# Optimization experiments

Measured on AMD Instinct MI355X. Metric: run time of the kernel, lower is better.

Reference implementation:

```python
import jax, jax.numpy as jnp
import numpy as np

B, L, D = 1, 4096, 1024
N_AR, N_DIFF, D_HEAD = 8, 8, 64
H = N_AR + N_DIFF
ROPE_BASE = 10000.0


def rotate_half(x):
    x1, x2 = jnp.split(x, 2, axis=-1)
    return jnp.concatenate([-x2, x1], axis=-1)


def rope_cos_sin(seq_len, d_head):
    inv_freq = 1.0 / (ROPE_BASE ** (jnp.arange(0, d_head, 2, dtype=jnp.float32) / d_head))
    t = jnp.arange(seq_len, dtype=jnp.float32)
    freqs = t[:, None] * inv_freq[None, :]          # [L, d_head//2]
    emb = jnp.concatenate([freqs, freqs], axis=-1)  # [L, d_head]
    return jnp.cos(emb), jnp.sin(emb)


def setup_inputs() -> dict:
    key = jax.random.key(0)
    ks = jax.random.split(key, 5)
    return {
        "hidden_states": jax.random.normal(ks[0], (B, L, D), dtype=jnp.float32),
        "Wq": jax.random.normal(ks[1], (D, H * D_HEAD), dtype=jnp.float32) * 0.02,
        "Wk": jax.random.normal(ks[2], (D, H * D_HEAD), dtype=jnp.float32) * 0.02,
        "Wv": jax.random.normal(ks[3], (D, H * D_HEAD), dtype=jnp.float32) * 0.02,
        "Wo": jax.random.normal(ks[4], (H * D_HEAD, D), dtype=jnp.float32) * 0.02,
    }


def _attend(q, k, v, mask):
    # q,k,v: [B, h, L, d]; mask: [L, L] additive
    scale = D_HEAD ** -0.5
    scores = jnp.einsum("bhqd,bhkd->bhqk", q, k) * scale + mask
    attn = jax.nn.softmax(scores.astype(jnp.float32), axis=-1).astype(q.dtype)
    return jnp.einsum("bhqk,bhkd->bhqd", attn, v)


def reference(hidden_states, Wq, Wk, Wv, Wo):
    b, l, _ = hidden_states.shape

    def heads(x, W):
        return (x @ W).reshape(b, l, H, D_HEAD).transpose(0, 2, 1, 3)  # [B,H,L,d]

    q = heads(hidden_states, Wq)
    k = heads(hidden_states, Wk)
    v = heads(hidden_states, Wv)

    cos, sin = rope_cos_sin(l, D_HEAD)  # [L, d]
    q = q * cos + rotate_half(q) * sin
    k = k * cos + rotate_half(k) * sin

    neg_inf = jnp.finfo(jnp.float32).min
    causal = jnp.where(jnp.tril(jnp.ones((l, l), dtype=bool)), 0.0, -jnp.inf).astype(jnp.float32)

    out_ar = _attend(q[:, :N_AR], k[:, :N_AR], v[:, :N_AR], causal)
    out_diff = _attend(q[:, N_AR:], k[:, N_AR:], v[:, N_AR:], jnp.zeros((l, l), jnp.float32))

    out = jnp.concatenate([out_ar, out_diff], axis=1)          # [B,H,L,d]
    out = out.transpose(0, 2, 1, 3).reshape(b, l, H * D_HEAD)  # [B,L,H*d]
    return out @ Wo
```

## Files before the change

kernel.cpp:

```cpp
#include <hip/hip_runtime.h>

#define LSEQ 4096
#define DMODEL 1024
#define HTOT 16
#define NAR 8
#define DHEAD 64
#define QKVS 3072

typedef unsigned short u16;
typedef unsigned int u32;
typedef __attribute__((ext_vector_type(8))) short bf16x8;
typedef __attribute__((ext_vector_type(4))) short bf16x4;
typedef __attribute__((ext_vector_type(4))) float f32x4;

typedef __attribute__((address_space(1))) void gvoid;
typedef __attribute__((address_space(3))) void lvoid;

__device__ __forceinline__ void cp16(const void* g, void* l) {
    __builtin_amdgcn_global_load_lds((gvoid*)(void*)g, (lvoid*)l, 16, 0, 0);
}

__device__ __forceinline__ float bfs(u16 v) { return __uint_as_float((u32)v << 16); }
__device__ __forceinline__ u16 f2bf(float f) {
    u32 x = __float_as_uint(f);
    return (u16)((x + 0x7fffu + ((x >> 16) & 1u)) >> 16);
}
__device__ __forceinline__ u32 pack2(float a, float b) {
    return (u32)f2bf(a) | ((u32)f2bf(b) << 16);
}

__global__ __launch_bounds__(256) void transp_cvt3(
    const float* __restrict__ Wq, const float* __restrict__ Wk,
    const float* __restrict__ Wv, u16* __restrict__ D)
{
    __shared__ u16 T[64][72];
    const float* S = (blockIdx.z == 0) ? Wq : ((blockIdx.z == 1) ? Wk : Wv);
    u16* Dz = D + (size_t)blockIdx.z * 1024 * 1024;
    const int tid = threadIdx.x;
    const int bx = blockIdx.x, by = blockIdx.y;
#pragma unroll
    for (int i = 0; i < 4; ++i) {
        int id = tid + i * 256;
        int fr = id >> 4, fc = id & 15;
        float4 v = *(const float4*)(S + (size_t)(by * 64 + fr) * 1024 + bx * 64 + fc * 4);
        T[fc * 4 + 0][fr] = f2bf(v.x);
        T[fc * 4 + 1][fr] = f2bf(v.y);
        T[fc * 4 + 2][fr] = f2bf(v.z);
        T[fc * 4 + 3][fr] = f2bf(v.w);
    }
    __syncthreads();
#pragma unroll
    for (int i = 0; i < 2; ++i) {
        int id = tid + i * 256;
        int c = id >> 3, g = id & 7;
        *(uint4*)(Dz + (size_t)(bx * 64 + c) * 1024 + by * 64 + g * 8) = *(const uint4*)&T[c][g * 8];
    }
}

__global__ __launch_bounds__(256) void transp_cvt(
    const float* __restrict__ S, u16* __restrict__ D)
{
    __shared__ u16 T[64][72];
    const int tid = threadIdx.x;
    const int bx = blockIdx.x, by = blockIdx.y;
#pragma unroll
    for (int i = 0; i < 4; ++i) {
        int id = tid + i * 256;
        int fr = id >> 4, fc = id & 15;
        float4 v = *(const float4*)(S + (size_t)(by * 64 + fr) * 1024 + bx * 64 + fc * 4);
        T[fc * 4 + 0][fr] = f2bf(v.x);
        T[fc * 4 + 1][fr] = f2bf(v.y);
        T[fc * 4 + 2][fr] = f2bf(v.z);
        T[fc * 4 + 3][fr] = f2bf(v.w);
    }
    __syncthreads();
#pragma unroll
    for (int i = 0; i < 2; ++i) {
        int id = tid + i * 256;
        int c = id >> 3, g = id & 7;
        *(uint4*)(D + (size_t)(bx * 64 + c) * 1024 + by * 64 + g * 8) = *(const uint4*)&T[c][g * 8];
    }
}

__global__ __launch_bounds__(256) void gemm_qkv(
    const float* __restrict__ A, const u16* __restrict__ Bt, u16* __restrict__ C)
{
    __shared__ u16 As[2][128][40];
    __shared__ u16 Bs[2][128][32];
    const int tid = threadIdx.x;
    const int lane = tid & 63, w = tid >> 6;
    const int col = lane & 15, quad = lane >> 4;
    const int bm = blockIdx.y << 7, bn = blockIdx.x << 7;
    const int wm = (w & 1) << 6, wn = (w >> 1) << 6;
    const int sr = lane >> 2, sc = (lane & 3) << 3;
    const int ar0 = tid >> 2, ag = (tid & 3) << 3;
    const f32x4 zero = {0.f, 0.f, 0.f, 0.f};
    f32x4 acc[4][4];
#pragma unroll
    for (int i = 0; i < 4; ++i)
#pragma unroll
        for (int j = 0; j < 4; ++j) acc[i][j] = zero;

    {
#pragma unroll
        for (int i = 0; i < 2; ++i)
            cp16(Bt + (size_t)(bn + w * 32 + i * 16 + sr) * 1024 + sc, &Bs[0][w * 32 + i * 16][0]);
        float4 a0[2], a1[2];
#pragma unroll
        for (int it = 0; it < 2; ++it) {
            const float* ap = A + (size_t)(bm + ar0 + it * 64) * 1024 + ag;
            a0[it] = *(const float4*)ap;
            a1[it] = *(const float4*)(ap + 4);
        }
#pragma unroll
        for (int it = 0; it < 2; ++it) {
            uint4 pk;
            pk.x = pack2(a0[it].x, a0[it].y); pk.y = pack2(a0[it].z, a0[it].w);
            pk.z = pack2(a1[it].x, a1[it].y); pk.w = pack2(a1[it].z, a1[it].w);
            *(uint4*)&As[0][ar0 + it * 64][ag] = pk;
        }
    }

    for (int kc = 0; kc < 32; ++kc) {
        const int cur = kc & 1, nxt = cur ^ 1;
        __syncthreads();
        const bool pre = (kc + 1 < 32);
        float4 a0[2], a1[2];
        if (pre) {
            const int k1 = (kc + 1) * 32;
#pragma unroll
            for (int i = 0; i < 2; ++i)
                cp16(Bt + (size_t)(bn + w * 32 + i * 16 + sr) * 1024 + k1 + sc,
                     &Bs[nxt][w * 32 + i * 16][0]);
#pragma unroll
            for (int it = 0; it < 2; ++it) {
                const float* ap = A + (size_t)(bm + ar0 + it * 64) * 1024 + k1 + ag;
                a0[it] = *(const float4*)ap;
                a1[it] = *(const float4*)(ap + 4);
            }
        }
        bf16x8 af[4], bfr[4];
#pragma unroll
        for (int i = 0; i < 4; ++i) af[i] = *(const bf16x8*)&As[cur][wm + i * 16 + col][quad * 8];
#pragma unroll
        for (int j = 0; j < 4; ++j) bfr[j] = *(const bf16x8*)&Bs[cur][wn + j * 16 + col][quad * 8];
#pragma unroll
        for (int i = 0; i < 4; ++i)
#pragma unroll
            for (int j = 0; j < 4; ++j)
                acc[i][j] = __builtin_amdgcn_mfma_f32_16x16x32_bf16(af[i], bfr[j], acc[i][j], 0, 0, 0);
        if (pre) {
#pragma unroll
            for (int it = 0; it < 2; ++it) {
                uint4 pk;
                pk.x = pack2(a0[it].x, a0[it].y); pk.y = pack2(a0[it].z, a0[it].w);
                pk.z = pack2(a1[it].x, a1[it].y); pk.w = pack2(a1[it].z, a1[it].w);
                *(uint4*)&As[nxt][ar0 + it * 64][ag] = pk;
            }
        }
    }
#pragma unroll
    for (int i = 0; i < 4; ++i)
#pragma unroll
        for (int j = 0; j < 4; ++j)
#pragma unroll
            for (int r = 0; r < 4; ++r)
                C[(size_t)(bm + wm + i * 16 + quad * 4 + r) * QKVS + bn + wn + j * 16 + col] =
                    f2bf(acc[i][j][r]);
}

__global__ __launch_bounds__(256) void gemm_out(
    const u16* __restrict__ A, const u16* __restrict__ Bt, float* __restrict__ C)
{
    __shared__ u16 As[2][128][32];
    __shared__ u16 Bs[2][128][32];
    const int tid = threadIdx.x;
    const int lane = tid & 63, w = tid >> 6;
    const int col = lane & 15, quad = lane >> 4;
    const int bm = blockIdx.y << 7, bn = blockIdx.x << 7;
    const int wm = (w & 1) << 6, wn = (w >> 1) << 6;
    const int sr = lane >> 2, sc = (lane & 3) << 3;
    const f32x4 zero = {0.f, 0.f, 0.f, 0.f};
    f32x4 acc[4][4];
#pragma unroll
    for (int i = 0; i < 4; ++i)
#pragma unroll
        for (int j = 0; j < 4; ++j) acc[i][j] = zero;

#pragma unroll
    for (int i = 0; i < 2; ++i) {
        const int r0 = w * 32 + i * 16;
        cp16(A  + (size_t)(bm + r0 + sr) * 1024 + sc, &As[0][r0][0]);
        cp16(Bt + (size_t)(bn + r0 + sr) * 1024 + sc, &Bs[0][r0][0]);
    }

    for (int kc = 0; kc < 32; ++kc) {
        const int cur = kc & 1, nxt = cur ^ 1;
        __syncthreads();
        if (kc + 1 < 32) {
            const int k1 = (kc + 1) * 32;
#pragma unroll
            for (int i = 0; i < 2; ++i) {
                const int r0 = w * 32 + i * 16;
                cp16(A  + (size_t)(bm + r0 + sr) * 1024 + k1 + sc, &As[nxt][r0][0]);
                cp16(Bt + (size_t)(bn + r0 + sr) * 1024 + k1 + sc, &Bs[nxt][r0][0]);
            }
        }
        bf16x8 af[4], bfr[4];
#pragma unroll
        for (int i = 0; i < 4; ++i) af[i] = *(const bf16x8*)&As[cur][wm + i * 16 + col][quad * 8];
#pragma unroll
        for (int j = 0; j < 4; ++j) bfr[j] = *(const bf16x8*)&Bs[cur][wn + j * 16 + col][quad * 8];
#pragma unroll
        for (int i = 0; i < 4; ++i)
#pragma unroll
            for (int j = 0; j < 4; ++j)
                acc[i][j] = __builtin_amdgcn_mfma_f32_16x16x32_bf16(af[i], bfr[j], acc[i][j], 0, 0, 0);
    }
#pragma unroll
    for (int i = 0; i < 4; ++i)
#pragma unroll
        for (int j = 0; j < 4; ++j)
#pragma unroll
            for (int r = 0; r < 4; ++r)
                C[(size_t)(bm + wm + i * 16 + quad * 4 + r) * 1024 + bn + wn + j * 16 + col] =
                    acc[i][j][r];
}

__global__ __launch_bounds__(256) void rope_kernel(u16* __restrict__ QKV)
{
    const int idx = blockIdx.x * 256 + threadIdx.x;
    const int i = idx & 31;
    const int h = (idx >> 5) & 15;
    const int t = idx >> 9;
    const float inv = __expf((float)i * -0.2878231366242557f);
    float s, c;
    __sincosf((float)t * inv, &s, &c);
    const size_t base = (size_t)t * QKVS + h * DHEAD + i;
    const float qs = 0.18033688011112042f;

    float q1 = bfs(QKV[base]), q2 = bfs(QKV[base + 32]);
    QKV[base]      = f2bf((q1 * c - q2 * s) * qs);
    QKV[base + 32] = f2bf((q2 * c + q1 * s) * qs);

    const size_t kb = base + 1024;
    float k1 = bfs(QKV[kb]), k2 = bfs(QKV[kb + 32]);
    QKV[kb]      = f2bf(k1 * c - k2 * s);
    QKV[kb + 32] = f2bf(k2 * c + k1 * s);
}

__global__ __launch_bounds__(256) void attn_mfma(
    const u16* __restrict__ QKV, u16* __restrict__ AO)
{
    __shared__ u16 Ks[2][64][64];
    __shared__ u16 Vt[2][64][72];
    const int bid = blockIdx.x;
    int h, qt;
    if (bid < 512) { h = 8 + (bid & 7); qt = bid >> 3; }
    else {
        int i = bid - 512; h = i & 7; int j = i >> 3;
        qt = (j & 1) ? (63 - (j >> 1)) : (j >> 1);
    }
    const bool causal = (h < NAR);
    const int tid = threadIdx.x;
    const int w = tid >> 6, lane = tid & 63;
    const int col = lane & 15, quad = lane >> 4;
    const int qb = qt * 64;
    const int qrow = qb + w * 16 + col;

    bf16x8 qf[2];
#pragma unroll
    for (int ks = 0; ks < 2; ++ks)
        qf[ks] = *(const bf16x8*)(QKV + (size_t)qrow * QKVS + h * DHEAD + ks * 32 + quad * 8);

    bf16x4 ones;
    ones[0] = (short)0x3F80; ones[1] = (short)0x3F80;
    ones[2] = (short)0x3F80; ones[3] = (short)0x3F80;

    const f32x4 zero = {0.f, 0.f, 0.f, 0.f};
    f32x4 O[5];
#pragma unroll
    for (int nd = 0; nd < 5; ++nd) O[nd] = zero;

    const int nch = causal ? (qt + 1) : (LSEQ / 64);
    const int kv_kp = tid & 31, kv_dg = tid >> 5;
    const int krow = lane >> 3;
    const int kcb = (lane & 7) ^ krow;
    const u16* kbase = QKV + (size_t)krow * QKVS + 1024 + h * DHEAD + kcb * 8;

    {
#pragma unroll
        for (int i = 0; i < 2; ++i)
            cp16(kbase + (size_t)((i * 4 + w) * 8) * QKVS, &Ks[0][(i * 4 + w) * 8][0]);
        const u16* vp = QKV + (size_t)(kv_kp * 2) * QKVS + 2048 + h * DHEAD + kv_dg * 8;
        bf16x8 v0 = *(const bf16x8*)vp;
        bf16x8 v1 = *(const bf16x8*)(vp + QKVS);
#pragma unroll
        for (int j = 0; j < 8; ++j)
            *(u32*)&Vt[0][kv_dg * 8 + j][kv_kp * 2] = (u32)(u16)v0[j] | ((u32)(u16)v1[j] << 16);
    }

    for (int ch = 0; ch < nch; ++ch) {
        const int cur = ch & 1, nxt = cur ^ 1;
        __syncthreads();
        const bool pre = (ch + 1 < nch);
        bf16x8 v0 = {}, v1 = {};
        if (pre) {
            const int c1 = (ch + 1) * 64;
#pragma unroll
            for (int i = 0; i < 2; ++i)
                cp16(kbase + (size_t)(c1 + (i * 4 + w) * 8) * QKVS, &Ks[nxt][(i * 4 + w) * 8][0]);
            const u16* vp = QKV + (size_t)(c1 + kv_kp * 2) * QKVS + 2048 + h * DHEAD + kv_dg * 8;
            v0 = *(const bf16x8*)vp;
            v1 = *(const bf16x8*)(vp + QKVS);
        }

        f32x4 st[4];
#pragma unroll
        for (int jn = 0; jn < 4; ++jn) st[jn] = zero;
#pragma unroll
        for (int jn = 0; jn < 4; ++jn)
#pragma unroll
            for (int ks = 0; ks < 2; ++ks) {
                bf16x8 kf = *(const bf16x8*)&Ks[cur][jn * 16 + col][((ks * 4 + quad) ^ (col & 7)) * 8];
                st[jn] = __builtin_amdgcn_mfma_f32_16x16x32_bf16(kf, qf[ks], st[jn], 0, 0, 0);
            }
        if (causal && ch * 64 + 63 > qb + w * 16) {
#pragma unroll
            for (int jn = 0; jn < 4; ++jn) {
                int kk = ch * 64 + jn * 16 + quad * 4;
#pragma unroll
                for (int r = 0; r < 4; ++r)
                    if (kk + r > qrow) st[jn][r] = -1e30f;
            }
        }
        bf16x4 pf[4];
#pragma unroll
        for (int jn = 0; jn < 4; ++jn) {
            pf[jn][0] = (short)f2bf(__builtin_amdgcn_exp2f(st[jn][0]));
            pf[jn][1] = (short)f2bf(__builtin_amdgcn_exp2f(st[jn][1]));
            pf[jn][2] = (short)f2bf(__builtin_amdgcn_exp2f(st[jn][2]));
            pf[jn][3] = (short)f2bf(__builtin_amdgcn_exp2f(st[jn][3]));
        }
#pragma unroll
        for (int nd = 0; nd < 4; ++nd)
#pragma unroll
            for (int jn = 0; jn < 4; ++jn) {
                bf16x4 vtf = *(const bf16x4*)&Vt[cur][nd * 16 + col][jn * 16 + quad * 4];
                O[nd] = __builtin_amdgcn_mfma_f32_16x16x16bf16_1k(vtf, pf[jn], O[nd], 0, 0, 0);
            }
#pragma unroll
        for (int jn = 0; jn < 4; ++jn)
            O[4] = __builtin_amdgcn_mfma_f32_16x16x16bf16_1k(ones, pf[jn], O[4], 0, 0, 0);

        if (pre) {
#pragma unroll
            for (int j = 0; j < 8; ++j)
                *(u32*)&Vt[nxt][kv_dg * 8 + j][kv_kp * 2] =
                    (u32)(u16)v0[j] | ((u32)(u16)v1[j] << 16);
        }
    }
    const float inv = 1.f / O[4][0];
#pragma unroll
    for (int nd = 0; nd < 4; ++nd) {
        ushort4 ov;
        ov.x = f2bf(O[nd][0] * inv);
        ov.y = f2bf(O[nd][1] * inv);
        ov.z = f2bf(O[nd][2] * inv);
        ov.w = f2bf(O[nd][3] * inv);
        *(ushort4*)(AO + (size_t)qrow * 1024 + h * DHEAD + nd * 16 + quad * 4) = ov;
    }
}

extern "C" void kernel_launch(void* const* d_in, const int* in_sizes, int n_in,
                              void* d_out, int out_size, void* d_ws, size_t ws_size,
                              hipStream_t stream)
{
    const float* X  = (const float*)d_in[0];
    const float* Wq = (const float*)d_in[1];
    const float* Wk = (const float*)d_in[2];
    const float* Wv = (const float*)d_in[3];
    const float* Wo = (const float*)d_in[4];
    float* out = (float*)d_out;

    u16* Wt  = (u16*)d_ws;
    u16* AOb = (u16*)d_ws;
    u16* QKV = (u16*)d_ws + (size_t)4 * 1024 * 1024;
    u16* Wot = QKV;

    transp_cvt3<<<dim3(16, 16, 3), 256, 0, stream>>>(Wq, Wk, Wv, Wt);
    gemm_qkv<<<dim3(24, 32), 256, 0, stream>>>(X, Wt, QKV);
    rope_kernel<<<(LSEQ * HTOT * 32) / 256, 256, 0, stream>>>(QKV);
    attn_mfma<<<1024, 256, 0, stream>>>(QKV, AOb);
    transp_cvt<<<dim3(16, 16), 256, 0, stream>>>(Wo, Wot);
    gemm_out<<<dim3(8, 32), 256, 0, stream>>>(AOb, Wot, out);
}
```

Before: 275.1 us.

## Double attention tile to 128 queries and 128 keys per block

The attention kernel now handles 128 query rows per block, with each wave doing two 16-row sub-tiles, and 128 keys per chunk. Each K/V fragment loaded from LDS is therefore reused across two query sub-tiles, which halves the number of blocks and the K/V global traffic per query. V is transposed with perm byte-shuffles, and probabilities are packed to bf16 by truncation instead of round-to-nearest. In exchange the kernel uses more registers and LDS, has half as many blocks (512 on a large GPU), and the causal blocks become coarser with more imbalance.

```diff
diff --git a/kernel.cpp b/kernel.cpp
--- a/kernel.cpp
+++ b/kernel.cpp
@@ -12,6 +12,7 @@
 typedef __attribute__((ext_vector_type(8))) short bf16x8;
 typedef __attribute__((ext_vector_type(4))) short bf16x4;
 typedef __attribute__((ext_vector_type(4))) float f32x4;
+typedef __attribute__((ext_vector_type(4))) unsigned int u32x4;
 
 typedef __attribute__((address_space(1))) void gvoid;
 typedef __attribute__((address_space(3))) void lvoid;
@@ -27,6 +28,9 @@
 }
 __device__ __forceinline__ u32 pack2(float a, float b) {
     return (u32)f2bf(a) | ((u32)f2bf(b) << 16);
+}
+__device__ __forceinline__ u32 packtr(float lo, float hi) {
+    return __builtin_amdgcn_perm(__float_as_uint(hi), __float_as_uint(lo), 0x07060302u);
 }
 
 __global__ __launch_bounds__(256) void transp_cvt3(
@@ -252,123 +256,156 @@
 __global__ __launch_bounds__(256) void attn_mfma(
     const u16* __restrict__ QKV, u16* __restrict__ AO)
 {
-    __shared__ u16 Ks[2][64][64];
-    __shared__ u16 Vt[2][64][72];
+    __shared__ u16 Ks[2][128][64];
+    __shared__ u16 Vt[2][64][136];
     const int bid = blockIdx.x;
     int h, qt;
-    if (bid < 512) { h = 8 + (bid & 7); qt = bid >> 3; }
-    else {
-        int i = bid - 512; h = i & 7; int j = i >> 3;
-        qt = (j & 1) ? (63 - (j >> 1)) : (j >> 1);
-    }
+    if (bid < 256) { h = 8 + (bid & 7); qt = bid >> 3; }
+    else { int i = bid - 256; h = i & 7; qt = 31 - (i >> 3); }
     const bool causal = (h < NAR);
     const int tid = threadIdx.x;
     const int w = tid >> 6, lane = tid & 63;
     const int col = lane & 15, quad = lane >> 4;
-    const int qb = qt * 64;
-    const int qrow = qb + w * 16 + col;
-
-    bf16x8 qf[2];
-#pragma unroll
-    for (int ks = 0; ks < 2; ++ks)
-        qf[ks] = *(const bf16x8*)(QKV + (size_t)qrow * QKVS + h * DHEAD + ks * 32 + quad * 8);
+    const int qb = qt * 128;
+    const int qr0 = qb + w * 32 + col;
+    const int qr1 = qr0 + 16;
+
+    bf16x8 qf[2][2];
+#pragma unroll
+    for (int s = 0; s < 2; ++s)
+#pragma unroll
+        for (int ks = 0; ks < 2; ++ks)
+            qf[s][ks] = *(const bf16x8*)(QKV + (size_t)(qr0 + s * 16) * QKVS +
+                                         h * DHEAD + ks * 32 + quad * 8);
 
     bf16x4 ones;
     ones[0] = (short)0x3F80; ones[1] = (short)0x3F80;
     ones[2] = (short)0x3F80; ones[3] = (short)0x3F80;
 
     const f32x4 zero = {0.f, 0.f, 0.f, 0.f};
-    f32x4 O[5];
-#pragma unroll
-    for (int nd = 0; nd < 5; ++nd) O[nd] = zero;
-
-    const int nch = causal ? (qt + 1) : (LSEQ / 64);
-    const int kv_kp = tid & 31, kv_dg = tid >> 5;
+    f32x4 O[2][5];
+#pragma unroll
+    for (int s = 0; s < 2; ++s)
+#pragma unroll
+        for (int nd = 0; nd < 5; ++nd) O[s][nd] = zero;
+
+    const int nch = causal ? (qt + 1) : (LSEQ / 128);
     const int krow = lane >> 3;
     const int kcb = (lane & 7) ^ krow;
     const u16* kbase = QKV + (size_t)krow * QKVS + 1024 + h * DHEAD + kcb * 8;
+    const u16* vbase = QKV + (size_t)(lane * 2) * QKVS + 2048 + h * DHEAD + w * 16;
 
     {
 #pragma unroll
-        for (int i = 0; i < 2; ++i)
+        for (int i = 0; i < 4; ++i)
             cp16(kbase + (size_t)((i * 4 + w) * 8) * QKVS, &Ks[0][(i * 4 + w) * 8][0]);
-        const u16* vp = QKV + (size_t)(kv_kp * 2) * QKVS + 2048 + h * DHEAD + kv_dg * 8;
-        bf16x8 v0 = *(const bf16x8*)vp;
-        bf16x8 v1 = *(const bf16x8*)(vp + QKVS);
-#pragma unroll
-        for (int j = 0; j < 8; ++j)
-            *(u32*)&Vt[0][kv_dg * 8 + j][kv_kp * 2] = (u32)(u16)v0[j] | ((u32)(u16)v1[j] << 16);
+        u32x4 A0 = *(u32x4*)(vbase);
+        u32x4 A1 = *(u32x4*)(vbase + 8);
+        u32x4 B0 = *(u32x4*)(vbase + QKVS);
+        u32x4 B1 = *(u32x4*)(vbase + QKVS + 8);
+#pragma unroll
+        for (int j = 0; j < 4; ++j) {
+            *(u32*)&Vt[0][w * 16 + 2 * j][lane * 2]     = __builtin_amdgcn_perm(B0[j], A0[j], 0x05040100u);
+            *(u32*)&Vt[0][w * 16 + 2 * j + 1][lane * 2] = __builtin_amdgcn_perm(B0[j], A0[j], 0x07060302u);
+            *(u32*)&Vt[0][w * 16 + 8 + 2 * j][lane * 2]     = __builtin_amdgcn_perm(B1[j], A1[j], 0x05040100u);
+            *(u32*)&Vt[0][w * 16 + 8 + 2 * j + 1][lane * 2] = __builtin_amdgcn_perm(B1[j], A1[j], 0x07060302u);
+        }
     }
 
     for (int ch = 0; ch < nch; ++ch) {
         const int cur = ch & 1, nxt = cur ^ 1;
         __syncthreads();
         const bool pre = (ch + 1 < nch);
-        bf16x8 v0 = {}, v1 = {};
+        u32x4 A0 = {}, A1 = {}, B0 = {}, B1 = {};
         if (pre) {
-            const int c1 = (ch + 1) * 64;
-#pragma unroll
-            for (int i = 0; i < 2; ++i)
-                cp16(kbase + (size_t)(c1 + (i * 4 + w) * 8) * QKVS, &Ks[nxt][(i * 4 + w) * 8][0]);
-            const u16* vp = QKV + (size_t)(c1 + kv_kp * 2) * QKVS + 2048 + h * DHEAD + kv_dg * 8;
-            v0 = *(const bf16x8*)vp;
-            v1 = *(const bf16x8*)(vp + QKVS);
-        }
-
-        f32x4 st[4];
-#pragma unroll
-        for (int jn = 0; jn < 4; ++jn) st[jn] = zero;
-#pragma unroll
-        for (int jn = 0; jn < 4; ++jn)
-#pragma unroll
-            for (int ks = 0; ks < 2; ++ks) {
-                bf16x8 kf = *(const bf16x8*)&Ks[cur][jn * 16 + col][((ks * 4 + quad) ^ (col & 7)) * 8];
-                st[jn] = __builtin_amdgcn_mfma_f32_16x16x32_bf16(kf, qf[ks], st[jn], 0, 0, 0);
-            }
-        if (causal && ch * 64 + 63 > qb + w * 16) {
-#pragma unroll
-            for (int jn = 0; jn < 4; ++jn) {
-                int kk = ch * 64 + jn * 16 + quad * 4;
-#pragma unroll
-                for (int r = 0; r < 4; ++r)
-                    if (kk + r > qrow) st[jn][r] = -1e30f;
-            }
-        }
-        bf16x4 pf[4];
-#pragma unroll
-        for (int jn = 0; jn < 4; ++jn) {
-            pf[jn][0] = (short)f2bf(__builtin_amdgcn_exp2f(st[jn][0]));
-            pf[jn][1] = (short)f2bf(__builtin_amdgcn_exp2f(st[jn][1]));
-            pf[jn][2] = (short)f2bf(__builtin_amdgcn_exp2f(st[jn][2]));
-            pf[jn][3] = (short)f2bf(__builtin_amdgcn_exp2f(st[jn][3]));
-        }
-#pragma unroll
-        for (int nd = 0; nd < 4; ++nd)
-#pragma unroll
-            for (int jn = 0; jn < 4; ++jn) {
-                bf16x4 vtf = *(const bf16x4*)&Vt[cur][nd * 16 + col][jn * 16 + quad * 4];
-                O[nd] = __builtin_amdgcn_mfma_f32_16x16x16bf16_1k(vtf, pf[jn], O[nd], 0, 0, 0);
-            }
-#pragma unroll
-        for (int jn = 0; jn < 4; ++jn)
-            O[4] = __builtin_amdgcn_mfma_f32_16x16x16bf16_1k(ones, pf[jn], O[4], 0, 0, 0);
+            const size_t c1 = (size_t)(ch + 1) * 128;
+#pragma unroll
+            for (int i = 0; i < 4; ++i)
+                cp16(kbase + (c1 + (i * 4 + w) * 8) * QKVS, &Ks[nxt][(i * 4 + w) * 8][0]);
+            const u16* vp = vbase + c1 * QKVS;
+            A0 = *(u32x4*)(vp);
+            A1 = *(u32x4*)(vp + 8);
+            B0 = *(u32x4*)(vp + QKVS);
+            B1 = *(u32x4*)(vp + QKVS + 8);
+        }
+
+#pragma unroll
+        for (int hf = 0; hf < 2; ++hf) {
+            f32x4 st[2][4];
+#pragma unroll
+            for (int s = 0; s < 2; ++s)
+#pragma unroll
+                for (int jj = 0; jj < 4; ++jj) st[s][jj] = zero;
+#pragma unroll
+            for (int jj = 0; jj < 4; ++jj)
+#pragma unroll
+                for (int ks = 0; ks < 2; ++ks) {
+                    bf16x8 kf = *(const bf16x8*)&Ks[cur][(hf * 4 + jj) * 16 + col]
+                                                    [((ks * 4 + quad) ^ (col & 7)) * 8];
+                    st[0][jj] = __builtin_amdgcn_mfma_f32_16x16x32_bf16(kf, qf[0][ks], st[0][jj], 0, 0, 0);
+                    st[1][jj] = __builtin_amdgcn_mfma_f32_16x16x32_bf16(kf, qf[1][ks], st[1][jj], 0, 0, 0);
+                }
+            if (causal && ch == qt) {
+#pragma unroll
+                for (int jj = 0; jj < 4; ++jj) {
+                    const int kk = ch * 128 + (hf * 4 + jj) * 16 + quad * 4;
+#pragma unroll
+                    for (int r = 0; r < 4; ++r) {
+                        if (kk + r > qr0) st[0][jj][r] = -1e30f;
+                        if (kk + r > qr1) st[1][jj][r] = -1e30f;
+                    }
+                }
+            }
+            bf16x4 pf[2][4];
+#pragma unroll
+            for (int s = 0; s < 2; ++s)
+#pragma unroll
+                for (int jj = 0; jj < 4; ++jj) {
+                    u32 lo = packtr(__builtin_amdgcn_exp2f(st[s][jj][0]),
+                                    __builtin_amdgcn_exp2f(st[s][jj][1]));
+                    u32 hi = packtr(__builtin_amdgcn_exp2f(st[s][jj][2]),
+                                    __builtin_amdgcn_exp2f(st[s][jj][3]));
+                    u32* p = (u32*)&pf[s][jj];
+                    p[0] = lo; p[1] = hi;
+                }
+#pragma unroll
+            for (int nd = 0; nd < 4; ++nd)
+#pragma unroll
+                for (int jj = 0; jj < 4; ++jj) {
+                    bf16x4 vtf = *(const bf16x4*)&Vt[cur][nd * 16 + col][(hf * 4 + jj) * 16 + quad * 4];
+                    O[0][nd] = __builtin_amdgcn_mfma_f32_16x16x16bf16_1k(vtf, pf[0][jj], O[0][nd], 0, 0, 0);
+                    O[1][nd] = __builtin_amdgcn_mfma_f32_16x16x16bf16_1k(vtf, pf[1][jj], O[1][nd], 0, 0, 0);
+                }
+#pragma unroll
+            for (int jj = 0; jj < 4; ++jj) {
+                O[0][4] = __builtin_amdgcn_mfma_f32_16x16x16bf16_1k(ones, pf[0][jj], O[0][4], 0, 0, 0);
+                O[1][4] = __builtin_amdgcn_mfma_f32_16x16x16bf16_1k(ones, pf[1][jj], O[1][4], 0, 0, 0);
+            }
+        }
 
         if (pre) {
 #pragma unroll
-            for (int j = 0; j < 8; ++j)
-                *(u32*)&Vt[nxt][kv_dg * 8 + j][kv_kp * 2] =
-                    (u32)(u16)v0[j] | ((u32)(u16)v1[j] << 16);
-        }
-    }
-    const float inv = 1.f / O[4][0];
-#pragma unroll
-    for (int nd = 0; nd < 4; ++nd) {
-        ushort4 ov;
-        ov.x = f2bf(O[nd][0] * inv);
-        ov.y = f2bf(O[nd][1] * inv);
-        ov.z = f2bf(O[nd][2] * inv);
-        ov.w = f2bf(O[nd][3] * inv);
-        *(ushort4*)(AO + (size_t)qrow * 1024 + h * DHEAD + nd * 16 + quad * 4) = ov;
+            for (int j = 0; j < 4; ++j) {
+                *(u32*)&Vt[nxt][w * 16 + 2 * j][lane * 2]     = __builtin_amdgcn_perm(B0[j], A0[j], 0x05040100u);
+                *(u32*)&Vt[nxt][w * 16 + 2 * j + 1][lane * 2] = __builtin_amdgcn_perm(B0[j], A0[j], 0x07060302u);
+                *(u32*)&Vt[nxt][w * 16 + 8 + 2 * j][lane * 2]     = __builtin_amdgcn_perm(B1[j], A1[j], 0x05040100u);
+                *(u32*)&Vt[nxt][w * 16 + 8 + 2 * j + 1][lane * 2] = __builtin_amdgcn_perm(B1[j], A1[j], 0x07060302u);
+            }
+        }
+    }
+#pragma unroll
+    for (int s = 0; s < 2; ++s) {
+        const float inv = 1.f / O[s][4][0];
+        const int qrow = qr0 + s * 16;
+#pragma unroll
+        for (int nd = 0; nd < 4; ++nd) {
+            ushort4 ov;
+            ov.x = f2bf(O[s][nd][0] * inv);
+            ov.y = f2bf(O[s][nd][1] * inv);
+            ov.z = f2bf(O[s][nd][2] * inv);
+            ov.w = f2bf(O[s][nd][3] * inv);
+            *(ushort4*)(AO + (size_t)qrow * 1024 + h * DHEAD + nd * 16 + quad * 4) = ov;
+        }
     }
 }
 
@@ -391,7 +428,7 @@
     transp_cvt3<<<dim3(16, 16, 3), 256, 0, stream>>>(Wq, Wk, Wv, Wt);
     gemm_qkv<<<dim3(24, 32), 256, 0, stream>>>(X, Wt, QKV);
     rope_kernel<<<(LSEQ * HTOT * 32) / 256, 256, 0, stream>>>(QKV);
-    attn_mfma<<<1024, 256, 0, stream>>>(QKV, AOb);
+    attn_mfma<<<512, 256, 0, stream>>>(QKV, AOb);
     transp_cvt<<<dim3(16, 16), 256, 0, stream>>>(Wo, Wot);
     gemm_out<<<dim3(8, 32), 256, 0, stream>>>(AOb, Wot, out);
 }
```

New measurement: 273.0 us. About the same (-0.8%).
